# Kernel optimization log

Measured on AMD Instinct MI355X. Metric: run time of the kernel, lower is better.

Reference implementation:

```python
import jax, jax.numpy as jnp
import numpy as np

D_MODEL = 1024
D_FF = 4096
NUM_EXPERTS = 8
TOP_K = 2
BATCH = 2
SEQ = 2048


def setup_inputs() -> dict:
    key = jax.random.key(0)
    ks = jax.random.split(key, 6)
    s_in = 1.0 / np.sqrt(D_MODEL)
    s_ff = 1.0 / np.sqrt(D_FF)
    return {
        "x": jax.random.normal(ks[0], (BATCH, SEQ, D_MODEL), dtype=jnp.float32),
        "gate_w": jax.random.normal(ks[1], (D_MODEL, NUM_EXPERTS), dtype=jnp.float32) * s_in,
        "w1": jax.random.normal(ks[2], (NUM_EXPERTS, D_MODEL, D_FF), dtype=jnp.float32) * s_in,
        "b1": jnp.zeros((NUM_EXPERTS, D_FF), dtype=jnp.float32),
        "w2": jax.random.normal(ks[3], (NUM_EXPERTS, D_FF, D_MODEL), dtype=jnp.float32) * s_ff,
        "b2": jnp.zeros((NUM_EXPERTS, D_MODEL), dtype=jnp.float32),
    }


def reference(x, gate_w, w1, b1, w2, b2):
    B, S, D = x.shape
    T = B * S
    # Router: logits -> softmax -> top-k -> renormalize selected weights
    router_logits = jnp.einsum("bsd,de->bse", x, gate_w)  # [B,S,E]
    probs = jax.nn.softmax(router_logits, axis=-1)
    top_k_weights, top_k_indices = jax.lax.top_k(probs, TOP_K)  # [B,S,K]
    top_k_weights = top_k_weights / jnp.sum(top_k_weights, axis=-1, keepdims=True)

    x_flat = x.reshape(T, D)
    # per-token, per-expert combine weight: sum over k of weight * (idx==e) -> [T,E]
    one_hot = jax.nn.one_hot(top_k_indices.reshape(T, TOP_K), NUM_EXPERTS, dtype=x.dtype)
    combine = jnp.einsum("tke,tk->te", one_hot, top_k_weights.reshape(T, TOP_K))

    # Dense grouped-GEMM over all experts (same math as masked gather/scatter loop,
    # since combine weight is zero for unselected experts)
    h = jnp.maximum(jnp.einsum("td,edf->etf", x_flat, w1) + b1[:, None, :], 0.0)  # [E,T,F]
    y = jnp.einsum("etf,efd->etd", h, w2) + b2[:, None, :]  # [E,T,D]
    out_flat = jnp.einsum("etd,te->td", y, combine)  # [T,D]
    output = out_flat.reshape(B, S, D)
    return output, router_logits, top_k_indices, top_k_weights
```

## Files before the change

### kernel.cpp

```cpp
#include <hip/hip_runtime.h>
#include <cstdint>
#include <cstddef>


#define D_MODEL 1024
#define D_FF    4096
#define NEXP    8
#define TOKENS  4096
#define SLOTS   8192
#define SLOTSP  9216

typedef __bf16 bf16x8 __attribute__((ext_vector_type(8)));
typedef float  f32x4  __attribute__((ext_vector_type(4)));

static __device__ __forceinline__ unsigned short f2bf(float f) {
  unsigned int u = __float_as_uint(f);
  u += 0x7fffu + ((u >> 16) & 1u);
  return (unsigned short)(u >> 16);
}

static __device__ __forceinline__ void async_ld16(const void* g, void* l) {
  __builtin_amdgcn_global_load_lds(
      (const __attribute__((address_space(1))) void*)g,
      (__attribute__((address_space(3))) void*)l, 16, 0, 0);
}


__global__ void init_kernel(int* __restrict__ tok_list) {
  const int g = blockIdx.x * 256 + threadIdx.x;
  if (g < SLOTSP) tok_list[g] = -1;
}

__global__ __launch_bounds__(256) void router_kernel(
    const float* __restrict__ x, const float* __restrict__ gw,
    float* __restrict__ out_logits, float* __restrict__ out_idx,
    float* __restrict__ out_w)
{
  const int w = threadIdx.x >> 6, lane = threadIdx.x & 63;
  const int t = blockIdx.x * 4 + w;
  float p[NEXP];
#pragma unroll
  for (int e = 0; e < NEXP; ++e) p[e] = 0.f;
  const float* xr = x + (size_t)t * D_MODEL;
#pragma unroll 4
  for (int i = 0; i < D_MODEL / 64; ++i) {
    const int d = i * 64 + lane;
    const float xv = xr[d];
    const float* g = gw + (size_t)d * NEXP;
#pragma unroll
    for (int e = 0; e < NEXP; ++e) p[e] += xv * g[e];
  }
#pragma unroll
  for (int e = 0; e < NEXP; ++e) {
#pragma unroll
    for (int s = 1; s < 64; s <<= 1) p[e] += __shfl_xor(p[e], s, 64);
  }
  if (lane == 0) {
    int i0 = 0;
#pragma unroll
    for (int e = 1; e < NEXP; ++e) if (p[e] > p[i0]) i0 = e;
    int i1 = (i0 == 0) ? 1 : 0;
#pragma unroll
    for (int e = 0; e < NEXP; ++e)
      if (e != i0 && p[e] > p[i1]) i1 = e;
    const float w0 = 1.f / (1.f + __expf(p[i1] - p[i0]));
#pragma unroll
    for (int e = 0; e < NEXP; ++e) out_logits[(size_t)t * NEXP + e] = p[e];
    out_idx[t * 2 + 0] = (float)i0;
    out_idx[t * 2 + 1] = (float)i1;
    out_w[t * 2 + 0] = w0;
    out_w[t * 2 + 1] = 1.f - w0;
  }
}

__global__ __launch_bounds__(256) void count_offsets_kernel(
    const float* __restrict__ out_idx, int* __restrict__ wsI)
{
  __shared__ int hist[NEXP];
  const int tid = threadIdx.x;
  if (tid < NEXP) hist[tid] = 0;
  if (tid < NEXP) wsI[8 + tid] = 0;
  __syncthreads();
  int c[NEXP];
#pragma unroll
  for (int e = 0; e < NEXP; ++e) c[e] = 0;
  for (int p = tid * 32; p < tid * 32 + 32; ++p) c[(int)out_idx[p]]++;
#pragma unroll
  for (int e = 0; e < NEXP; ++e) if (c[e]) atomicAdd(&hist[e], c[e]);
  __syncthreads();
  if (tid == 0) {
    int s = 0, nb = 0;
    for (int e = 0; e < NEXP; ++e) {
      wsI[16 + e] = s;
      const int nblk = (hist[e] + 127) >> 7;
      for (int j = 0; j < nblk; ++j) {
        wsI[32 + nb] = e;
        wsI[128 + nb] = s + j * 128;
        ++nb;
      }
      s += nblk << 7;
    }
    wsI[16 + NEXP] = s;
    wsI[25] = nb;
  }
}

__global__ void scatter_kernel(const float* __restrict__ out_idx,
                               int* __restrict__ cursor,
                               const int* __restrict__ po,
                               int* __restrict__ pair_slot,
                               int* __restrict__ tok_list)
{
  const int p = blockIdx.x * 256 + threadIdx.x;
  const int lane = threadIdx.x & 63;
  const int e = (int)out_idx[p];
  int pos = 0;
#pragma unroll
  for (int e8 = 0; e8 < NEXP; ++e8) {
    const unsigned long long m = __ballot(e == e8);
    if (m) {
      const int leader = __ffsll((long long)m) - 1;
      int base = 0;
      if (lane == leader) base = atomicAdd(&cursor[e8], (int)__popcll(m));
      base = __shfl(base, leader, 64);
      if (e == e8)
        pos = po[e8] + base +
              (int)__popcll(m & ((1ull << lane) - 1ull));
    }
  }
  tok_list[pos] = p >> 1;
  pair_slot[p] = pos;
}

__global__ __launch_bounds__(256) void gather_cvt(
    const float* __restrict__ x, const int* __restrict__ tok_list,
    unsigned short* __restrict__ xg)
{
  const int gid = blockIdx.x * 256 + threadIdx.x;
  const int row = gid >> 7, seg = gid & 127;
  const int tok = tok_list[row];
  if (tok < 0) return;
  const float* src = x + (size_t)tok * D_MODEL + seg * 8;
  const float4 a = *(const float4*)(src);
  const float4 b = *(const float4*)(src + 4);
  ushort4 lo = make_ushort4(f2bf(a.x), f2bf(a.y), f2bf(a.z), f2bf(a.w));
  ushort4 hi = make_ushort4(f2bf(b.x), f2bf(b.y), f2bf(b.z), f2bf(b.w));
  unsigned short* d = xg + (size_t)row * D_MODEL + seg * 8;
  *(ushort4*)(d) = lo;
  *(ushort4*)(d + 4) = hi;
}

__global__ __launch_bounds__(256) void transpose_cvt(
    const float* __restrict__ src, unsigned short* __restrict__ dst,
    int K, int N)
{
  const int e = blockIdx.z;
  const int n0 = blockIdx.x * 64;
  const int k0 = blockIdx.y * 64;
  __shared__ float t[64][65];
  const int c4 = (threadIdx.x & 15) * 4;
  const int r  = threadIdx.x >> 4;
  const float* s = src + (size_t)e * K * N + (size_t)k0 * N + n0;
#pragma unroll
  for (int i = 0; i < 4; ++i) {
    const float4 v = *(const float4*)(s + (size_t)(r + 16 * i) * N + c4);
    t[r + 16 * i][c4 + 0] = v.x;
    t[r + 16 * i][c4 + 1] = v.y;
    t[r + 16 * i][c4 + 2] = v.z;
    t[r + 16 * i][c4 + 3] = v.w;
  }
  __syncthreads();
  unsigned short* d = dst + (size_t)e * N * K + (size_t)n0 * K + k0;
#pragma unroll
  for (int i = 0; i < 4; ++i) {
    const int n = r + 16 * i;
    ushort4 v;
    v.x = f2bf(t[c4 + 0][n]);
    v.y = f2bf(t[c4 + 1][n]);
    v.z = f2bf(t[c4 + 2][n]);
    v.w = f2bf(t[c4 + 3][n]);
    *(ushort4*)(d + (size_t)n * K + c4) = v;
  }
}

template <int RELU>
__global__ __launch_bounds__(256) void gemm_mfma(
    const unsigned short* __restrict__ A, const unsigned short* __restrict__ Bt,
    const float* __restrict__ bias, void* __restrict__ Cout,
    const int* __restrict__ wsI, int K, int N)
{
  const int gx = gridDim.x;
  const int nwg = gx * gridDim.y;
  const int cpx = nwg >> 3;
  int f = blockIdx.y * gx + blockIdx.x;
  f = (f & 7) * cpx + (f >> 3);
  const int bx = f % gx;
  const int by = f / gx;

  if (by >= wsI[25]) return;
  const int e   = wsI[32 + by];
  const int gr0 = wsI[128 + by];
  const int col0 = bx * 128;

  const int klen = K / gridDim.z;
  const int kbeg = blockIdx.z * klen;
  const int kend = kbeg + klen;

  __shared__ unsigned short ldsA[128 * 64];
  __shared__ unsigned short ldsB[128 * 64];

  const int tid = threadIdx.x;
  const int lane = tid & 63;
  const int w = tid >> 6;
  const int wr = w >> 1, wc = w & 1;
  const int m15 = lane & 15, q = lane >> 4;

  f32x4 zero = {0.f, 0.f, 0.f, 0.f};
  f32x4 acc[4][4];
#pragma unroll
  for (int mt = 0; mt < 4; ++mt)
#pragma unroll
    for (int nt = 0; nt < 4; ++nt) acc[mt][nt] = zero;

  const size_t off0 = (size_t)(tid >> 3) * K + ((tid & 7) ^ ((tid >> 3) & 7)) * 8;
  const size_t jstep = (size_t)32 * K;
  const unsigned short* Abase = A + (size_t)gr0 * K;
  const unsigned short* Bbase = Bt + (size_t)e * N * K + (size_t)col0 * K;

  const int sw = q ^ (m15 & 7);

  for (int kk = kbeg; kk < kend; kk += 64) {
#pragma unroll
    for (int j = 0; j < 4; ++j) {
      async_ld16(Abase + off0 + j * jstep + kk, &ldsA[(j * 256 + tid) * 8]);
      async_ld16(Bbase + off0 + j * jstep + kk, &ldsB[(j * 256 + tid) * 8]);
    }
    __syncthreads();
#pragma unroll
    for (int ks2 = 0; ks2 < 2; ++ks2) {
      const int slot8 = (sw ^ (ks2 << 2)) * 8;
      bf16x8 af[4], bf[4];
#pragma unroll
      for (int mt = 0; mt < 4; ++mt)
        af[mt] = *(const bf16x8*)&ldsA[(wr * 64 + mt * 16 + m15) * 64 + slot8];
#pragma unroll
      for (int nt = 0; nt < 4; ++nt)
        bf[nt] = *(const bf16x8*)&ldsB[(wc * 64 + nt * 16 + m15) * 64 + slot8];
#pragma unroll
      for (int mt = 0; mt < 4; ++mt)
#pragma unroll
        for (int nt = 0; nt < 4; ++nt)
          acc[mt][nt] = __builtin_amdgcn_mfma_f32_16x16x32_bf16(
              af[mt], bf[nt], acc[mt][nt], 0, 0, 0);
    }
    __syncthreads();
  }

  const size_t zoff = (size_t)blockIdx.z * SLOTSP * (size_t)N;
#pragma unroll
  for (int nt = 0; nt < 4; ++nt) {
    const int c = col0 + wc * 64 + nt * 16 + m15;
    const float bv = (blockIdx.z == 0) ? bias[(size_t)e * N + c] : 0.f;
#pragma unroll
    for (int mt = 0; mt < 4; ++mt) {
      const size_t rbase = (size_t)(gr0 + wr * 64 + mt * 16 + q * 4);
      if (RELU) {
        unsigned short* Cp = (unsigned short*)Cout;
#pragma unroll
        for (int i = 0; i < 4; ++i)
          Cp[(rbase + i) * N + c] = f2bf(fmaxf(acc[mt][nt][i] + bv, 0.f));
      } else {
        float* Cp = (float*)Cout + zoff;
#pragma unroll
        for (int i = 0; i < 4; ++i)
          Cp[(rbase + i) * N + c] = acc[mt][nt][i] + bv;
      }
    }
  }
}

__global__ __launch_bounds__(256) void combine_kernel(
    const float* __restrict__ y, const int* __restrict__ pair_slot,
    const float* __restrict__ out_w, float* __restrict__ out)
{
  const int gid = blockIdx.x * 256 + threadIdx.x;
  if (gid >= TOKENS * (D_MODEL / 4)) return;
  const int t = gid >> 8;
  const int qd = gid & 255;
  const float w0 = out_w[t * 2 + 0], w1 = out_w[t * 2 + 1];
  const int p0 = pair_slot[t * 2 + 0], p1 = pair_slot[t * 2 + 1];
  const float* y1 = y + (size_t)SLOTSP * D_MODEL;
  const float4 a0 = *(const float4*)(y  + (size_t)p0 * D_MODEL + qd * 4);
  const float4 a1 = *(const float4*)(y1 + (size_t)p0 * D_MODEL + qd * 4);
  const float4 b0 = *(const float4*)(y  + (size_t)p1 * D_MODEL + qd * 4);
  const float4 b1 = *(const float4*)(y1 + (size_t)p1 * D_MODEL + qd * 4);
  float4 o;
  o.x = w0 * (a0.x + a1.x) + w1 * (b0.x + b1.x);
  o.y = w0 * (a0.y + a1.y) + w1 * (b0.y + b1.y);
  o.z = w0 * (a0.z + a1.z) + w1 * (b0.z + b1.z);
  o.w = w0 * (a0.w + a1.w) + w1 * (b0.w + b1.w);
  *(float4*)(out + (size_t)t * D_MODEL + qd * 4) = o;
}

extern "C" void kernel_launch(void* const* d_in, const int* in_sizes, int n_in,
                              void* d_out, int out_size, void* d_ws, size_t ws_size,
                              hipStream_t stream)
{
  (void)in_sizes; (void)n_in; (void)out_size; (void)ws_size;
  const float* x  = (const float*)d_in[0];
  const float* gw = (const float*)d_in[1];
  const float* w1 = (const float*)d_in[2];
  const float* b1 = (const float*)d_in[3];
  const float* w2 = (const float*)d_in[4];
  const float* b2 = (const float*)d_in[5];

  float* out        = (float*)d_out;
  float* out_logits = out + (size_t)TOKENS * D_MODEL;
  float* out_idx    = out_logits + (size_t)TOKENS * NEXP;
  float* out_w      = out_idx + (size_t)TOKENS * 2;

  int* wsI       = (int*)d_ws;
  int* po        = wsI + 16;
  int* tok_list  = wsI + 512;
  int* pair_slot = wsI + 10240;
  unsigned short* xg  = (unsigned short*)((char*)d_ws + (1 << 17));
  unsigned short* w1t = xg  + (size_t)SLOTSP * D_MODEL;
  unsigned short* w2t = w1t + (size_t)NEXP * D_FF * D_MODEL;
  unsigned short* h   = w2t + (size_t)NEXP * D_MODEL * D_FF;
  float*          y   = (float*)xg;

  init_kernel<<<SLOTSP / 256, 256, 0, stream>>>(tok_list);
  router_kernel<<<TOKENS / 4, 256, 0, stream>>>(x, gw, out_logits, out_idx, out_w);
  count_offsets_kernel<<<1, 256, 0, stream>>>(out_idx, wsI);
  scatter_kernel<<<SLOTS / 256, 256, 0, stream>>>(out_idx, wsI + 8, po, pair_slot, tok_list);
  gather_cvt<<<SLOTSP * 128 / 256, 256, 0, stream>>>(x, tok_list, xg);
  transpose_cvt<<<dim3(D_FF / 64, D_MODEL / 64, NEXP), 256, 0, stream>>>(w1, w1t, D_MODEL, D_FF);
  transpose_cvt<<<dim3(D_MODEL / 64, D_FF / 64, NEXP), 256, 0, stream>>>(w2, w2t, D_FF, D_MODEL);
  gemm_mfma<1><<<dim3(D_FF / 128, 72, 1), 256, 0, stream>>>(
      xg, w1t, b1, (void*)h, wsI, D_MODEL, D_FF);
  gemm_mfma<0><<<dim3(D_MODEL / 128, 72, 2), 256, 0, stream>>>(
      h, w2t, b2, (void*)y, wsI, D_FF, D_MODEL);
  combine_kernel<<<(TOKENS * D_MODEL / 4) / 256, 256, 0, stream>>>(
      y, pair_slot, out_w, out);
}
```

Measured before the change: 594.8 us.

## Fuse fp32 weight loading and bf16 conversion into GEMM, dropping transpose kernels

Removes the two separate transpose/convert passes over w1 and w2. Each GEMM block now reads the fp32 weights directly, converts them to bf16 in registers and writes them in the swizzled layout into LDS. The goal is to stop reading and writing the full weight tensors in an extra pass per call. The trade-off is that every M-tile re-reads fp32 weights (twice the bytes of bf16) through synchronous strided loads instead of async LDS loads, which may stall the GEMM main loop. Separately, the tok_list initialisation is folded into count_offsets, whose counting loop becomes coalesced, and y gets its own buffer instead of aliasing xg.

```diff
diff --git a/kernel.cpp b/kernel.cpp
--- a/kernel.cpp
+++ b/kernel.cpp
@@ -25,11 +25,6 @@
       (__attribute__((address_space(3))) void*)l, 16, 0, 0);
 }
 
-
-__global__ void init_kernel(int* __restrict__ tok_list) {
-  const int g = blockIdx.x * 256 + threadIdx.x;
-  if (g < SLOTSP) tok_list[g] = -1;
-}
 
 __global__ __launch_bounds__(256) void router_kernel(
     const float* __restrict__ x, const float* __restrict__ gw,
@@ -74,17 +69,19 @@
 }
 
 __global__ __launch_bounds__(256) void count_offsets_kernel(
-    const float* __restrict__ out_idx, int* __restrict__ wsI)
+    const float* __restrict__ out_idx, int* __restrict__ wsI,
+    int* __restrict__ tok_list)
 {
   __shared__ int hist[NEXP];
   const int tid = threadIdx.x;
+  for (int i = tid; i < SLOTSP; i += 256) tok_list[i] = -1;
   if (tid < NEXP) hist[tid] = 0;
   if (tid < NEXP) wsI[8 + tid] = 0;
   __syncthreads();
   int c[NEXP];
 #pragma unroll
   for (int e = 0; e < NEXP; ++e) c[e] = 0;
-  for (int p = tid * 32; p < tid * 32 + 32; ++p) c[(int)out_idx[p]]++;
+  for (int p = tid; p < SLOTS; p += 256) c[(int)out_idx[p]]++;
 #pragma unroll
   for (int e = 0; e < NEXP; ++e) if (c[e]) atomicAdd(&hist[e], c[e]);
   __syncthreads();
@@ -150,42 +147,9 @@
   *(ushort4*)(d + 4) = hi;
 }
 
-__global__ __launch_bounds__(256) void transpose_cvt(
-    const float* __restrict__ src, unsigned short* __restrict__ dst,
-    int K, int N)
-{
-  const int e = blockIdx.z;
-  const int n0 = blockIdx.x * 64;
-  const int k0 = blockIdx.y * 64;
-  __shared__ float t[64][65];
-  const int c4 = (threadIdx.x & 15) * 4;
-  const int r  = threadIdx.x >> 4;
-  const float* s = src + (size_t)e * K * N + (size_t)k0 * N + n0;
-#pragma unroll
-  for (int i = 0; i < 4; ++i) {
-    const float4 v = *(const float4*)(s + (size_t)(r + 16 * i) * N + c4);
-    t[r + 16 * i][c4 + 0] = v.x;
-    t[r + 16 * i][c4 + 1] = v.y;
-    t[r + 16 * i][c4 + 2] = v.z;
-    t[r + 16 * i][c4 + 3] = v.w;
-  }
-  __syncthreads();
-  unsigned short* d = dst + (size_t)e * N * K + (size_t)n0 * K + k0;
-#pragma unroll
-  for (int i = 0; i < 4; ++i) {
-    const int n = r + 16 * i;
-    ushort4 v;
-    v.x = f2bf(t[c4 + 0][n]);
-    v.y = f2bf(t[c4 + 1][n]);
-    v.z = f2bf(t[c4 + 2][n]);
-    v.w = f2bf(t[c4 + 3][n]);
-    *(ushort4*)(d + (size_t)n * K + c4) = v;
-  }
-}
-
 template <int RELU>
 __global__ __launch_bounds__(256) void gemm_mfma(
-    const unsigned short* __restrict__ A, const unsigned short* __restrict__ Bt,
+    const unsigned short* __restrict__ A, const float* __restrict__ W,
     const float* __restrict__ bias, void* __restrict__ Cout,
     const int* __restrict__ wsI, int K, int N)
 {
@@ -225,15 +189,32 @@
   const size_t off0 = (size_t)(tid >> 3) * K + ((tid & 7) ^ ((tid >> 3) & 7)) * 8;
   const size_t jstep = (size_t)32 * K;
   const unsigned short* Abase = A + (size_t)gr0 * K;
-  const unsigned short* Bbase = Bt + (size_t)e * N * K + (size_t)col0 * K;
+
+  const int nloc = tid & 63;
+  const int wv = tid >> 6;
+  const float* Wc0 = W + (size_t)e * K * N + (col0 + nloc);
 
   const int sw = q ^ (m15 & 7);
 
   for (int kk = kbeg; kk < kend; kk += 64) {
 #pragma unroll
-    for (int j = 0; j < 4; ++j) {
+    for (int j = 0; j < 4; ++j)
       async_ld16(Abase + off0 + j * jstep + kk, &ldsA[(j * 256 + tid) * 8]);
-      async_ld16(Bbase + off0 + j * jstep + kk, &ldsB[(j * 256 + tid) * 8]);
+#pragma unroll
+    for (int jo = 0; jo < 2; ++jo) {
+#pragma unroll
+      for (int jn = 0; jn < 2; ++jn) {
+        const int o = wv + 4 * jo;
+        const int nrow = nloc + 64 * jn;
+        const float* p = Wc0 + 64 * jn + (size_t)(kk + o * 8) * N;
+        float fv[8];
+#pragma unroll
+        for (int i = 0; i < 8; ++i) fv[i] = p[i * N];
+        bf16x8 bv;
+#pragma unroll
+        for (int i = 0; i < 8; ++i) bv[i] = (__bf16)fv[i];
+        *(bf16x8*)&ldsB[nrow * 64 + ((o ^ (nrow & 7)) * 8)] = bv;
+      }
     }
     __syncthreads();
 #pragma unroll
@@ -323,23 +304,18 @@
   int* po        = wsI + 16;
   int* tok_list  = wsI + 512;
   int* pair_slot = wsI + 10240;
-  unsigned short* xg  = (unsigned short*)((char*)d_ws + (1 << 17));
-  unsigned short* w1t = xg  + (size_t)SLOTSP * D_MODEL;
-  unsigned short* w2t = w1t + (size_t)NEXP * D_FF * D_MODEL;
-  unsigned short* h   = w2t + (size_t)NEXP * D_MODEL * D_FF;
-  float*          y   = (float*)xg;
-
-  init_kernel<<<SLOTSP / 256, 256, 0, stream>>>(tok_list);
+  unsigned short* xg = (unsigned short*)((char*)d_ws + (1 << 17));
+  unsigned short* h  = xg + (size_t)SLOTSP * D_MODEL;
+  float*          y  = (float*)(h + (size_t)SLOTSP * D_FF);
+
   router_kernel<<<TOKENS / 4, 256, 0, stream>>>(x, gw, out_logits, out_idx, out_w);
-  count_offsets_kernel<<<1, 256, 0, stream>>>(out_idx, wsI);
+  count_offsets_kernel<<<1, 256, 0, stream>>>(out_idx, wsI, tok_list);
   scatter_kernel<<<SLOTS / 256, 256, 0, stream>>>(out_idx, wsI + 8, po, pair_slot, tok_list);
   gather_cvt<<<SLOTSP * 128 / 256, 256, 0, stream>>>(x, tok_list, xg);
-  transpose_cvt<<<dim3(D_FF / 64, D_MODEL / 64, NEXP), 256, 0, stream>>>(w1, w1t, D_MODEL, D_FF);
-  transpose_cvt<<<dim3(D_MODEL / 64, D_FF / 64, NEXP), 256, 0, stream>>>(w2, w2t, D_FF, D_MODEL);
   gemm_mfma<1><<<dim3(D_FF / 128, 72, 1), 256, 0, stream>>>(
-      xg, w1t, b1, (void*)h, wsI, D_MODEL, D_FF);
+      xg, w1, b1, (void*)h, wsI, D_MODEL, D_FF);
   gemm_mfma<0><<<dim3(D_MODEL / 128, 72, 2), 256, 0, stream>>>(
-      h, w2t, b2, (void*)y, wsI, D_FF, D_MODEL);
+      h, w2, b2, (void*)y, wsI, D_FF, D_MODEL);
   combine_kernel<<<(TOKENS * D_MODEL / 4) / 256, 256, 0, stream>>>(
       y, pair_slot, out_w, out);
 }
```

Result: no change. 596.1 us (+0.2%).
